# Performance work log

Hardware: AMD Instinct MI355X
Metric: run time of the kernel (lower is better)

The kernel has to match this reference:

```python
import jax, jax.numpy as jnp
import numpy as np

QMAX = 127.0  # int8 symmetric range per get_quant_min_max(torch.int8)


def setup_inputs() -> dict:
    key = jax.random.key(0)
    k1, k2, k3, k4, k5, k6 = jax.random.split(key, 6)
    B, S, IN, OUT = 4, 2048, 4096, 4096
    x = jax.random.normal(k1, (B, S, IN), dtype=jnp.float32)
    # smoothquant-style per-input-channel scale (1/scale in torch code), positive
    input_scale = jax.random.uniform(k2, (IN,), jnp.float32, 0.5, 2.0)
    # per-tensor static activation scale (positive scalar)
    act_scale = jax.random.uniform(k3, (), jnp.float32, 0.01, 0.03)
    # pre-quantized int8 weight values in [-127, 127], stored as int32
    w_int = jax.random.randint(k4, (OUT, IN), -127, 128, dtype=jnp.int32)
    # per-out-channel weight scale
    w_scale = jax.random.uniform(k5, (OUT,), jnp.float32, 0.001, 0.01)
    bias = jax.random.normal(k6, (OUT,), dtype=jnp.float32) * 0.1
    return {"x": x, "input_scale": input_scale, "act_scale": act_scale,
            "w_int": w_int, "w_scale": w_scale, "bias": bias}


def reference(x, input_scale, act_scale, w_int, w_scale, bias):
    # mode == 'quantized' path of QModule.forward with forward_module = F.linear
    # 1) smooth-scale activations, 2) static affine int8 quantize (zero_point NONE)
    xs = x * input_scale  # [B,S,IN]
    xi = jnp.clip(jnp.round(xs / act_scale), -QMAX, QMAX).astype(jnp.int32)
    # 3) integer matmul (exact, matches torch double matmul of int values + round)
    acc = jnp.einsum('bsi,oi->bso', xi, w_int)  # int32 accumulate, exact
    # 4) dequant: scale = q(q(scale_i * scale_w, f32), f32) -> plain f32 product here
    scale = act_scale * w_scale  # [OUT]
    out = acc.astype(jnp.float32) * scale + bias
    return out
```

## Files before the change

### kernel.cpp

```cpp
#include <hip/hip_runtime.h>
#include <hip/hip_bf16.h>
#include <stdint.h>

#define Mdim 8192
#define Ndim 4096
#define Kdim 4096

#define BM 128
#define BN 128
#define BK 128

typedef int v4i __attribute__((ext_vector_type(4)));

__device__ __forceinline__ void gload_lds16(const void* g, void* l) {
  __builtin_amdgcn_global_load_lds(
      (const __attribute__((address_space(1))) unsigned int*)g,
      (__attribute__((address_space(3))) unsigned int*)l,
      16 , 0 , 0 );
}

__global__ void quant_x_kernel(const float* __restrict__ x,
                               const float* __restrict__ in_scale,
                               const float* __restrict__ act_scale_p,
                               int8_t* __restrict__ xq) {
  const float inv_act = 1.0f / (*act_scale_p);
  const int64_t tid = (int64_t)blockIdx.x * blockDim.x + threadIdx.x;
  const int64_t base = tid * 16;
  const int k0 = (int)(base & (Kdim - 1));
  const float4* xv = (const float4*)(x + base);
  const float4* sv = (const float4*)(in_scale + k0);
  alignas(16) int8_t ob[16];
#pragma unroll
  for (int j = 0; j < 4; ++j) {
    float4 xx = xv[j];
    float4 ss = sv[j];
    float r0 = rintf((xx.x * ss.x) * inv_act);
    float r1 = rintf((xx.y * ss.y) * inv_act);
    float r2 = rintf((xx.z * ss.z) * inv_act);
    float r3 = rintf((xx.w * ss.w) * inv_act);
    r0 = fminf(fmaxf(r0, -127.f), 127.f);
    r1 = fminf(fmaxf(r1, -127.f), 127.f);
    r2 = fminf(fmaxf(r2, -127.f), 127.f);
    r3 = fminf(fmaxf(r3, -127.f), 127.f);
    ob[j * 4 + 0] = (int8_t)r0;
    ob[j * 4 + 1] = (int8_t)r1;
    ob[j * 4 + 2] = (int8_t)r2;
    ob[j * 4 + 3] = (int8_t)r3;
  }
  *(v4i*)(xq + base) = *(const v4i*)ob;
}

__global__ void pack_w_kernel(const int* __restrict__ w, int8_t* __restrict__ wq) {
  const int64_t tid = (int64_t)blockIdx.x * blockDim.x + threadIdx.x;
  const int64_t base = tid * 16;
  const int4* wv = (const int4*)(w + base);
  alignas(16) int8_t ob[16];
#pragma unroll
  for (int j = 0; j < 4; ++j) {
    int4 t = wv[j];
    ob[j * 4 + 0] = (int8_t)t.x;
    ob[j * 4 + 1] = (int8_t)t.y;
    ob[j * 4 + 2] = (int8_t)t.z;
    ob[j * 4 + 3] = (int8_t)t.w;
  }
  *(v4i*)(wq + base) = *(const v4i*)ob;
}

__global__ __launch_bounds__(256) void gemm_i8_kernel(
    const int8_t* __restrict__ Aq, const int8_t* __restrict__ Bq,
    const float* __restrict__ w_scale, const float* __restrict__ bias,
    const float* __restrict__ act_scale_p, float* __restrict__ out) {
  __shared__ alignas(16) int8_t As[2][BM * 64];
  __shared__ alignas(16) int8_t Bs[2][BN * 64];

  const int t = threadIdx.x;

  const int lin = blockIdx.x;
  const int within = lin & 63;
  const int m_blk = (lin >> 6) * 2 + (within & 1);
  const int n_blk = within >> 1;
  const int m0 = m_blk * BM;
  const int n0 = n_blk * BN;

  const int srow = t >> 2;
  const int scol = ((t & 3) ^ ((t >> 3) & 3)) * 16;
  const int8_t* gA0 = Aq + (int64_t)(m0 + srow) * Kdim + scol;
  const int8_t* gA1 = gA0 + (int64_t)64 * Kdim;
  const int8_t* gB0 = Bq + (int64_t)(n0 + srow) * Kdim + scol;
  const int8_t* gB1 = gB0 + (int64_t)64 * Kdim;

  const int w = t >> 6;
  const int l = t & 63;
  const int wm = (w >> 1) * 64;
  const int wn = (w & 1) * 64;
  const int lrow = l & 15;
  const int lk = (((l >> 4) ^ ((l >> 1) & 3))) * 16;

  v4i acc[4][4] = {};

  for (int kt = 0; kt < Kdim; kt += BK) {
#pragma unroll
    for (int h = 0; h < 2; ++h) {
      const int ko = kt + h * 64;
      gload_lds16(gA0 + ko, As[h] + t * 16);
      gload_lds16(gA1 + ko, As[h] + 4096 + t * 16);
      gload_lds16(gB0 + ko, Bs[h] + t * 16);
      gload_lds16(gB1 + ko, Bs[h] + 4096 + t * 16);
    }
    __syncthreads();

#pragma unroll
    for (int h = 0; h < 2; ++h) {
      v4i af[4], bf[4];
#pragma unroll
      for (int i = 0; i < 4; ++i) {
        af[i] = *(const v4i*)(As[h] + (wm + i * 16 + lrow) * 64 + lk);
        bf[i] = *(const v4i*)(Bs[h] + (wn + i * 16 + lrow) * 64 + lk);
      }
#pragma unroll
      for (int i = 0; i < 4; ++i) {
#pragma unroll
        for (int j = 0; j < 4; ++j) {
          acc[i][j] = __builtin_amdgcn_mfma_i32_16x16x64_i8(af[i], bf[j], acc[i][j], 0, 0, 0);
        }
      }
    }
    __syncthreads();
  }

  const float act = *act_scale_p;
  const int rowbase = (l >> 4) * 4;
#pragma unroll
  for (int j = 0; j < 4; ++j) {
    const int n = n0 + wn + j * 16 + lrow;
    const float sc = act * w_scale[n];
    const float bs = bias[n];
#pragma unroll
    for (int i = 0; i < 4; ++i) {
      const int mb = m0 + wm + i * 16 + rowbase;
#pragma unroll
      for (int r = 0; r < 4; ++r) {
        out[(int64_t)(mb + r) * Ndim + n] = (float)acc[i][j][r] * sc + bs;
      }
    }
  }
}

extern "C" void kernel_launch(void* const* d_in, const int* in_sizes, int n_in,
                              void* d_out, int out_size, void* d_ws, size_t ws_size,
                              hipStream_t stream) {
  const float* x        = (const float*)d_in[0];
  const float* in_scale = (const float*)d_in[1];
  const float* actp     = (const float*)d_in[2];
  const int*   w_int    = (const int*)d_in[3];
  const float* w_scale  = (const float*)d_in[4];
  const float* bias     = (const float*)d_in[5];
  float* out = (float*)d_out;

  int8_t* Aq = (int8_t*)d_ws;
  int8_t* Bq = (int8_t*)d_ws + (size_t)Mdim * Kdim;

  {
    const int64_t nthreads = (int64_t)Mdim * Kdim / 16;
    quant_x_kernel<<<(int)(nthreads / 256), 256, 0, stream>>>(x, in_scale, actp, Aq);
  }
  {
    const int64_t nthreads = (int64_t)Ndim * Kdim / 16;
    pack_w_kernel<<<(int)(nthreads / 256), 256, 0, stream>>>(w_int, Bq);
  }
  {
    gemm_i8_kernel<<<dim3(2048), 256, 0, stream>>>(Aq, Bq, w_scale, bias, actp, out);
  }
}
```

Before: 428.6 us.

## Use 256x256 tiles with 8 waves and a ping-pong prefetch pipeline

```diff
diff --git a/kernel.cpp b/kernel.cpp
--- a/kernel.cpp
+++ b/kernel.cpp
@@ -6,8 +6,8 @@
 #define Ndim 4096
 #define Kdim 4096
 
-#define BM 128
-#define BN 128
+#define BM 256
+#define BN 256
 #define BK 128
 
 typedef int v4i __attribute__((ext_vector_type(4)));
@@ -66,18 +66,39 @@
   *(v4i*)(wq + base) = *(const v4i*)ob;
 }
 
-__global__ __launch_bounds__(256) void gemm_i8_kernel(
+#define PBAR()                        \
+  do {                                \
+    asm volatile("" ::: "memory");    \
+    __builtin_amdgcn_s_barrier();     \
+    asm volatile("" ::: "memory");    \
+  } while (0)
+#define LGKM0() asm volatile("s_waitcnt lgkmcnt(0)" ::: "memory")
+#define VMCNT(n) asm volatile("s_waitcnt vmcnt(" #n ")" ::: "memory")
+
+#define MFMA16(mh)                                                        \
+  do {                                                                    \
+    __builtin_amdgcn_s_setprio(1);                                        \
+    _Pragma("unroll") for (int i = 0; i < 4; ++i) {                       \
+      _Pragma("unroll") for (int j = 0; j < 4; ++j) {                     \
+        acc[(mh) * 4 + i][j] = __builtin_amdgcn_mfma_i32_16x16x64_i8(     \
+            af[i], bf[j], acc[(mh) * 4 + i][j], 0, 0, 0);                 \
+      }                                                                   \
+    }                                                                     \
+    __builtin_amdgcn_s_setprio(0);                                        \
+  } while (0)
+
+__global__ __launch_bounds__(512, 2) void gemm_i8_kernel(
     const int8_t* __restrict__ Aq, const int8_t* __restrict__ Bq,
     const float* __restrict__ w_scale, const float* __restrict__ bias,
     const float* __restrict__ act_scale_p, float* __restrict__ out) {
-  __shared__ alignas(16) int8_t As[2][BM * 64];
-  __shared__ alignas(16) int8_t Bs[2][BN * 64];
+  __shared__ alignas(16) int8_t As[2][2][BM * 64];
+  __shared__ alignas(16) int8_t Bs[2][2][BN * 64];
 
   const int t = threadIdx.x;
 
   const int lin = blockIdx.x;
-  const int within = lin & 63;
-  const int m_blk = (lin >> 6) * 2 + (within & 1);
+  const int within = lin & 31;
+  const int m_blk = (lin >> 5) * 2 + (within & 1);
   const int n_blk = within >> 1;
   const int m0 = m_blk * BM;
   const int n0 = n_blk * BN;
@@ -85,48 +106,75 @@
   const int srow = t >> 2;
   const int scol = ((t & 3) ^ ((t >> 3) & 3)) * 16;
   const int8_t* gA0 = Aq + (int64_t)(m0 + srow) * Kdim + scol;
-  const int8_t* gA1 = gA0 + (int64_t)64 * Kdim;
+  const int8_t* gA1 = gA0 + (int64_t)128 * Kdim;
   const int8_t* gB0 = Bq + (int64_t)(n0 + srow) * Kdim + scol;
-  const int8_t* gB1 = gB0 + (int64_t)64 * Kdim;
+  const int8_t* gB1 = gB0 + (int64_t)128 * Kdim;
+  const int ldst = t * 16;
 
   const int w = t >> 6;
   const int l = t & 63;
-  const int wm = (w >> 1) * 64;
-  const int wn = (w & 1) * 64;
+  const int wm = (w >> 2) * 128;
+  const int wn = (w & 3) * 64;
   const int lrow = l & 15;
-  const int lk = (((l >> 4) ^ ((l >> 1) & 3))) * 16;
-
-  v4i acc[4][4] = {};
+  const int lk = ((l >> 4) ^ ((l >> 1) & 3)) * 16;
+  const int abase = (wm + lrow) * 64 + lk;
+  const int bbase = (wn + lrow) * 64 + lk;
+
+  v4i acc[8][4] = {};
+
+#define STG(MAT, buf, ks, h, koff) \
+  gload_lds16(g##MAT##h + (koff) + (ks) * 64, &MAT##s[buf][ks][(h) * 8192 + ldst])
+
+  STG(A, 0, 0, 0, 0); STG(B, 0, 0, 0, 0);
+  STG(A, 0, 0, 1, 0); STG(B, 0, 0, 1, 0);
+  STG(A, 0, 1, 0, 0); STG(B, 0, 1, 0, 0);
+  STG(A, 0, 1, 1, 0); STG(B, 0, 1, 1, 0);
+  VMCNT(4);
+  PBAR();
 
   for (int kt = 0; kt < Kdim; kt += BK) {
-#pragma unroll
-    for (int h = 0; h < 2; ++h) {
-      const int ko = kt + h * 64;
-      gload_lds16(gA0 + ko, As[h] + t * 16);
-      gload_lds16(gA1 + ko, As[h] + 4096 + t * 16);
-      gload_lds16(gB0 + ko, Bs[h] + t * 16);
-      gload_lds16(gB1 + ko, Bs[h] + 4096 + t * 16);
-    }
-    __syncthreads();
-
-#pragma unroll
-    for (int h = 0; h < 2; ++h) {
-      v4i af[4], bf[4];
-#pragma unroll
-      for (int i = 0; i < 4; ++i) {
-        af[i] = *(const v4i*)(As[h] + (wm + i * 16 + lrow) * 64 + lk);
-        bf[i] = *(const v4i*)(Bs[h] + (wn + i * 16 + lrow) * 64 + lk);
-      }
-#pragma unroll
-      for (int i = 0; i < 4; ++i) {
-#pragma unroll
-        for (int j = 0; j < 4; ++j) {
-          acc[i][j] = __builtin_amdgcn_mfma_i32_16x16x64_i8(af[i], bf[j], acc[i][j], 0, 0, 0);
-        }
-      }
-    }
-    __syncthreads();
-  }
+    const int cur = (kt >> 7) & 1;
+    const int nxt = cur ^ 1;
+    int kn = kt + BK;
+    if (kn >= Kdim) kn = 0;
+
+    v4i af[4], bf[4];
+
+#pragma unroll
+    for (int j = 0; j < 4; ++j) bf[j] = *(const v4i*)&Bs[cur][0][bbase + j * 1024];
+#pragma unroll
+    for (int i = 0; i < 4; ++i) af[i] = *(const v4i*)&As[cur][0][abase + i * 1024];
+    STG(A, nxt, 0, 0, kn); STG(B, nxt, 0, 0, kn);
+    PBAR(); LGKM0();
+    MFMA16(0);
+    PBAR();
+
+#pragma unroll
+    for (int i = 0; i < 4; ++i) af[i] = *(const v4i*)&As[cur][0][abase + 4096 + i * 1024];
+    STG(A, nxt, 0, 1, kn); STG(B, nxt, 0, 1, kn);
+    PBAR(); LGKM0();
+    MFMA16(1);
+    VMCNT(4);
+    PBAR();
+
+#pragma unroll
+    for (int j = 0; j < 4; ++j) bf[j] = *(const v4i*)&Bs[cur][1][bbase + j * 1024];
+#pragma unroll
+    for (int i = 0; i < 4; ++i) af[i] = *(const v4i*)&As[cur][1][abase + i * 1024];
+    STG(A, nxt, 1, 0, kn); STG(B, nxt, 1, 0, kn);
+    PBAR(); LGKM0();
+    MFMA16(0);
+    PBAR();
+
+#pragma unroll
+    for (int i = 0; i < 4; ++i) af[i] = *(const v4i*)&As[cur][1][abase + 4096 + i * 1024];
+    STG(A, nxt, 1, 1, kn); STG(B, nxt, 1, 1, kn);
+    PBAR(); LGKM0();
+    MFMA16(1);
+    VMCNT(4);
+    PBAR();
+  }
+  VMCNT(0);
 
   const float act = *act_scale_p;
   const int rowbase = (l >> 4) * 4;
@@ -136,7 +184,7 @@
     const float sc = act * w_scale[n];
     const float bs = bias[n];
 #pragma unroll
-    for (int i = 0; i < 4; ++i) {
+    for (int i = 0; i < 8; ++i) {
       const int mb = m0 + wm + i * 16 + rowbase;
 #pragma unroll
       for (int r = 0; r < 4; ++r) {
@@ -169,6 +217,6 @@
     pack_w_kernel<<<(int)(nthreads / 256), 256, 0, stream>>>(w_int, Bq);
   }
   {
-    gemm_i8_kernel<<<dim3(2048), 256, 0, stream>>>(Aq, Bq, w_scale, bias, actp, out);
-  }
-}
+    gemm_i8_kernel<<<dim3(512), 512, 0, stream>>>(Aq, Bq, w_scale, bias, actp, out);
+  }
+}
```

New measurement: 403.2 us. 5.9% less time.

## Replace LDS-staged GEMM with direct-to-register loads and 256x256 tiles

Applied to the files above, without the earlier changes.

```diff
diff --git a/kernel.cpp b/kernel.cpp
--- a/kernel.cpp
+++ b/kernel.cpp
@@ -6,18 +6,7 @@
 #define Ndim 4096
 #define Kdim 4096
 
-#define BM 128
-#define BN 128
-#define BK 128
-
 typedef int v4i __attribute__((ext_vector_type(4)));
-
-__device__ __forceinline__ void gload_lds16(const void* g, void* l) {
-  __builtin_amdgcn_global_load_lds(
-      (const __attribute__((address_space(1))) unsigned int*)g,
-      (__attribute__((address_space(3))) unsigned int*)l,
-      16 , 0 , 0 );
-}
 
 __global__ void quant_x_kernel(const float* __restrict__ x,
                                const float* __restrict__ in_scale,
@@ -66,66 +55,66 @@
   *(v4i*)(wq + base) = *(const v4i*)ob;
 }
 
-__global__ __launch_bounds__(256) void gemm_i8_kernel(
+__global__ __launch_bounds__(512, 2) void gemm_i8_kernel(
     const int8_t* __restrict__ Aq, const int8_t* __restrict__ Bq,
     const float* __restrict__ w_scale, const float* __restrict__ bias,
     const float* __restrict__ act_scale_p, float* __restrict__ out) {
-  __shared__ alignas(16) int8_t As[2][BM * 64];
-  __shared__ alignas(16) int8_t Bs[2][BN * 64];
-
   const int t = threadIdx.x;
 
   const int lin = blockIdx.x;
-  const int within = lin & 63;
-  const int m_blk = (lin >> 6) * 2 + (within & 1);
+  const int within = lin & 31;
+  const int m_blk = (lin >> 5) * 2 + (within & 1);
   const int n_blk = within >> 1;
-  const int m0 = m_blk * BM;
-  const int n0 = n_blk * BN;
-
-  const int srow = t >> 2;
-  const int scol = ((t & 3) ^ ((t >> 3) & 3)) * 16;
-  const int8_t* gA0 = Aq + (int64_t)(m0 + srow) * Kdim + scol;
-  const int8_t* gA1 = gA0 + (int64_t)64 * Kdim;
-  const int8_t* gB0 = Bq + (int64_t)(n0 + srow) * Kdim + scol;
-  const int8_t* gB1 = gB0 + (int64_t)64 * Kdim;
+  const int m0 = m_blk * 256;
+  const int n0 = n_blk * 256;
 
   const int w = t >> 6;
   const int l = t & 63;
-  const int wm = (w >> 1) * 64;
-  const int wn = (w & 1) * 64;
+  const int wm = (w >> 2) * 128;
+  const int wn = (w & 3) * 64;
   const int lrow = l & 15;
-  const int lk = (((l >> 4) ^ ((l >> 1) & 3))) * 16;
+  const int kch = (l >> 4) * 16;
 
-  v4i acc[4][4] = {};
+  const int8_t* Ab = Aq + (int64_t)(m0 + wm + lrow) * Kdim + kch;
+  const int8_t* Bb = Bq + (int64_t)(n0 + wn + lrow) * Kdim + kch;
 
-  for (int kt = 0; kt < Kdim; kt += BK) {
-#pragma unroll
-    for (int h = 0; h < 2; ++h) {
-      const int ko = kt + h * 64;
-      gload_lds16(gA0 + ko, As[h] + t * 16);
-      gload_lds16(gA1 + ko, As[h] + 4096 + t * 16);
-      gload_lds16(gB0 + ko, Bs[h] + t * 16);
-      gload_lds16(gB1 + ko, Bs[h] + 4096 + t * 16);
-    }
-    __syncthreads();
+  v4i acc[8][4] = {};
+  v4i a0[8], b0[4], a1[8], b1[4];
 
-#pragma unroll
-    for (int h = 0; h < 2; ++h) {
-      v4i af[4], bf[4];
-#pragma unroll
-      for (int i = 0; i < 4; ++i) {
-        af[i] = *(const v4i*)(As[h] + (wm + i * 16 + lrow) * 64 + lk);
-        bf[i] = *(const v4i*)(Bs[h] + (wn + i * 16 + lrow) * 64 + lk);
-      }
-#pragma unroll
-      for (int i = 0; i < 4; ++i) {
-#pragma unroll
-        for (int j = 0; j < 4; ++j) {
-          acc[i][j] = __builtin_amdgcn_mfma_i32_16x16x64_i8(af[i], bf[j], acc[i][j], 0, 0, 0);
-        }
-      }
-    }
-    __syncthreads();
+#define LDA(dst, koff)                                                     \
+  do {                                                                     \
+    _Pragma("unroll") for (int i = 0; i < 8; ++i)                          \
+        dst[i] = *(const v4i*)(Ab + (int64_t)i * (16 * Kdim) + (koff));    \
+  } while (0)
+#define LDB(dst, koff)                                                     \
+  do {                                                                     \
+    _Pragma("unroll") for (int j = 0; j < 4; ++j)                          \
+        dst[j] = *(const v4i*)(Bb + (int64_t)j * (16 * Kdim) + (koff));    \
+  } while (0)
+#define MFMA32(AS, BS)                                                     \
+  do {                                                                     \
+    __builtin_amdgcn_s_setprio(1);                                         \
+    _Pragma("unroll") for (int i = 0; i < 8; ++i) {                        \
+      _Pragma("unroll") for (int j = 0; j < 4; ++j) {                      \
+        acc[i][j] = __builtin_amdgcn_mfma_i32_16x16x64_i8(                 \
+            AS[i], BS[j], acc[i][j], 0, 0, 0);                             \
+      }                                                                    \
+    }                                                                      \
+    __builtin_amdgcn_s_setprio(0);                                         \
+  } while (0)
+
+  LDA(a0, 0);
+  LDB(b0, 0);
+
+  for (int ks = 0; ks < Kdim; ks += 128) {
+    LDA(a1, ks + 64);
+    LDB(b1, ks + 64);
+    MFMA32(a0, b0);
+
+    const int k2 = (ks + 128 < Kdim) ? (ks + 128) : 0;
+    LDA(a0, k2);
+    LDB(b0, k2);
+    MFMA32(a1, b1);
   }
 
   const float act = *act_scale_p;
@@ -136,7 +125,7 @@
     const float sc = act * w_scale[n];
     const float bs = bias[n];
 #pragma unroll
-    for (int i = 0; i < 4; ++i) {
+    for (int i = 0; i < 8; ++i) {
       const int mb = m0 + wm + i * 16 + rowbase;
 #pragma unroll
       for (int r = 0; r < 4; ++r) {
@@ -169,6 +158,6 @@
     pack_w_kernel<<<(int)(nthreads / 256), 256, 0, stream>>>(w_int, Bq);
   }
   {
-    gemm_i8_kernel<<<dim3(2048), 256, 0, stream>>>(Aq, Bq, w_scale, bias, actp, out);
+    gemm_i8_kernel<<<dim3(512), 512, 0, stream>>>(Aq, Bq, w_scale, bias, actp, out);
   }
 }
```

Result: slower. 618.6 us (+44.3%).
